# Performance work log

Measured on AMD Instinct MI355X. Metric: run time of the kernel, lower is better.

The kernel has to match this reference:

```python
import jax, jax.numpy as jnp
import numpy as np

B = 256        # batch_size
T = 256        # max_length
H = 1024       # hidden width (hardcoded in module)
NOISE = 128    # noise_depth
NOUT = 100     # n_outputs
EPS = 1e-5     # BatchNorm1d default eps
SLOPE = 0.01   # LeakyReLU default negative_slope


def _bn(x, g, b):
    # BatchNorm1d in training mode: biased batch stats over dim 0
    m = jnp.mean(x, axis=0)
    v = jnp.var(x, axis=0)
    return (x - m) * jax.lax.rsqrt(v + EPS) * g + b


def setup_inputs() -> dict:
    key = jax.random.key(0)
    ks = jax.random.split(key, 16)
    s = 0.02
    d = {
        "z": jax.random.normal(ks[0], (B, NOISE), jnp.float32),
        # projection linears (torch Linear weight layout: [out, in])
        "W_zh": jax.random.normal(ks[1], (H, NOISE), jnp.float32) * s,
        "b_zh": jnp.zeros((H,), jnp.float32),
        "W_zc": jax.random.normal(ks[2], (H, NOISE), jnp.float32) * s,
        "b_zc": jnp.zeros((H,), jnp.float32),
        # BN affine params (torch default init: gamma=1, beta=0)
        "g_bnzh": jnp.ones((H,), jnp.float32), "b_bnzh": jnp.zeros((H,), jnp.float32),
        "g_bnzc": jnp.ones((H,), jnp.float32), "b_bnzc": jnp.zeros((H,), jnp.float32),
        # LSTMCell params, gate order i,f,g,o
        "W_ih": jax.random.normal(ks[3], (4 * H, H), jnp.float32) * s,
        "b_ih": jnp.zeros((4 * H,), jnp.float32),
        "W_hh": jax.random.normal(ks[4], (4 * H, H), jnp.float32) * s,
        "b_hh": jnp.zeros((4 * H,), jnp.float32),
        "g_bn0": jnp.ones((H,), jnp.float32), "b_bn0": jnp.zeros((H,), jnp.float32),
        "W1": jax.random.normal(ks[5], (512, H), jnp.float32) * s,
        "b1": jnp.zeros((512,), jnp.float32),
        "g_bn1": jnp.ones((512,), jnp.float32), "b_bn1": jnp.zeros((512,), jnp.float32),
        "W2": jax.random.normal(ks[6], (256, 512), jnp.float32) * s,
        "b2": jnp.zeros((256,), jnp.float32),
        "g_bn2": jnp.ones((256,), jnp.float32), "b_bn2": jnp.zeros((256,), jnp.float32),
        "W3": jax.random.normal(ks[7], (NOUT, 256), jnp.float32) * s,
        "b3": jnp.zeros((NOUT,), jnp.float32),
        # 'go' token: one-hot [1,0,...,0] tiled over batch
        "go": jnp.zeros((B, H), jnp.float32).at[:, 0].set(1.0),
    }
    return d


def reference(z, W_zh, b_zh, W_zc, b_zc, g_bnzh, b_bnzh, g_bnzc, b_bnzc,
              W_ih, b_ih, W_hh, b_hh, g_bn0, b_bn0, W1, b1, g_bn1, b_bn1,
              W2, b2, g_bn2, b_bn2, W3, b3, go):
    zh = _bn(z @ W_zh.T + b_zh, g_bnzh, b_bnzh)   # initial h
    zc = _bn(z @ W_zc.T + b_zc, g_bnzc, b_bnzc)   # initial c

    def step(carry, _):
        h, c, x = carry
        gates = x @ W_ih.T + b_ih + h @ W_hh.T + b_hh  # [B, 4H]
        i, f, g, o = jnp.split(gates, 4, axis=1)
        c2 = jax.nn.sigmoid(f) * c + jax.nn.sigmoid(i) * jnp.tanh(g)
        h2 = jax.nn.sigmoid(o) * jnp.tanh(c2)
        return (h2, c2, h2), h2  # next input is h2 (out = hx)

    _, ys = jax.lax.scan(step, (zh, zc, go), None, length=T)  # ys: [T, B, H]

    # torch: output = stack(dim=2) -> [B, H, T]; then view(-1, H) on raw memory
    output = jnp.transpose(ys, (1, 2, 0))          # [B, H, T] contiguous
    output_stack = output.reshape(-1, H)           # faithful raw reshape (mixes H and T)

    o1 = jax.nn.leaky_relu(_bn(output_stack, g_bn0, b_bn0) @ W1.T + b1, SLOPE)
    o2 = jax.nn.leaky_relu(_bn(o1, g_bn1, b_bn1) @ W2.T + b2, SLOPE)
    o3 = _bn(o2, g_bn2, b_bn2) @ W3.T + b3          # [B*T*?, NOUT] flat

    output_unstack = o3.reshape(B, -1, T)           # [B, NOUT, T]
    return jax.nn.softmax(output_unstack, axis=1)
```

## Files before the change

kernel.cpp:

```cpp
#include <hip/hip_runtime.h>
#include <hip/hip_bf16.h>

typedef __attribute__((ext_vector_type(8))) short bf16x8;
typedef __attribute__((ext_vector_type(4))) float f32x4;

#define NBLK 256

__device__ inline unsigned short f2b(float x){
  union { float f; unsigned int u; } v; v.f = x;
  unsigned int u = v.u;
  return (unsigned short)((u + 0x7FFFu + ((u >> 16) & 1u)) >> 16);
}
__device__ inline float b2f(unsigned short h){
  union { unsigned int u; float f; } v; v.u = ((unsigned int)h) << 16; return v.f;
}
__device__ inline float sigm(float x){ return 1.f / (1.f + __expf(-x)); }
__device__ inline float tanh_f(float x){ float e2 = __expf(2.f * x); return 1.f - 2.f / (e2 + 1.f); }

__global__ __launch_bounds__(256) void zerofill(float* __restrict__ p, int n){
  int i = blockIdx.x * 256 + threadIdx.x;
  if (i < n) p[i] = 0.f;
}

__device__ inline int packrow(int n){
  int g = n >> 10, h = n & 1023;
  return (h >> 3) * 32 + (h & 7) * 4 + g;
}

__global__ __launch_bounds__(256) void prep_w(
    const float* __restrict__ Wih, const float* __restrict__ Whh,
    const float* __restrict__ bih, const float* __restrict__ bhh,
    unsigned short* __restrict__ Wsum_p, unsigned short* __restrict__ Whh_b,
    float* __restrict__ bias_sp)
{
  size_t idx = (size_t)blockIdx.x * 256 + threadIdx.x;
  int n = (int)(idx >> 10), k = (int)(idx & 1023);
  int g = n >> 10, h = n & 1023;
  float wi = Wih[idx], wh = Whh[idx];
  int htile = h >> 3;
  int r  = ((h & 7) << 2) | g;
  int nt = r >> 4, lr2 = r & 15;
  int kb = k >> 5, lg2 = (k >> 3) & 3, e = k & 7;
  size_t dest = (size_t)htile * 32768 + (size_t)nt * 16384 + (size_t)kb * 512
              + (size_t)(lg2 * 16 + lr2) * 8 + e;
  Wsum_p[dest] = f2b(wi + wh);
  Whh_b[idx] = f2b(wh);
  if (idx < 4096) bias_sp[packrow((int)idx)] = bih[idx] + bhh[idx];
}

__global__ __launch_bounds__(256) void prep_b0(
    const float* __restrict__ Wih, const float* __restrict__ go,
    const float* __restrict__ bih, const float* __restrict__ bhh,
    float* __restrict__ bias0)
{
  __shared__ float red[4];
  int n = blockIdx.x, t = threadIdx.x;
  float acc = 0.f;
  for (int k = t; k < 1024; k += 256) acc += Wih[(size_t)n*1024 + k] * go[k];
  for (int off = 32; off > 0; off >>= 1) acc += __shfl_down(acc, off, 64);
  if ((t & 63) == 0) red[t >> 6] = acc;
  __syncthreads();
  if (t == 0) bias0[n] = bih[n] + bhh[n] + red[0] + red[1] + red[2] + red[3];
}

__global__ __launch_bounds__(256) void zproj(
    const float* __restrict__ z, const float* __restrict__ Wzh, const float* __restrict__ bzh,
    const float* __restrict__ Wzc, const float* __restrict__ bzc,
    float* __restrict__ zh_raw, float* __restrict__ zc_raw)
{
  int idx = blockIdx.x * 256 + threadIdx.x;
  int b = idx >> 10, c = idx & 1023;
  const float* zr = z + b * 128;
  const float* wh = Wzh + c * 128;
  const float* wc = Wzc + c * 128;
  float s1 = bzh[c], s2 = bzc[c];
  #pragma unroll 8
  for (int k = 0; k < 128; k++){ float zv = zr[k]; s1 += zv * wh[k]; s2 += zv * wc[k]; }
  zh_raw[idx] = s1; zc_raw[idx] = s2;
}

__global__ __launch_bounds__(256) void bn_init(
    const float* __restrict__ zh_raw, const float* __restrict__ zc_raw,
    const float* __restrict__ g_h, const float* __restrict__ bt_h,
    const float* __restrict__ g_c, const float* __restrict__ bt_c,
    unsigned short* __restrict__ zh_b, float* __restrict__ c_f)
{
  __shared__ float red[4][4];
  int c = blockIdx.x, r = threadIdx.x;
  float v1 = zh_raw[r * 1024 + c];
  float v2 = zc_raw[r * 1024 + c];
  float s[4] = { v1, v1*v1, v2, v2*v2 };
  #pragma unroll
  for (int i = 0; i < 4; i++){
    float x = s[i];
    for (int off = 32; off > 0; off >>= 1) x += __shfl_down(x, off, 64);
    if ((r & 63) == 0) red[i][r >> 6] = x;
  }
  __syncthreads();
  float m1 = (red[0][0]+red[0][1]+red[0][2]+red[0][3]) * (1.f/256.f);
  float q1 = (red[1][0]+red[1][1]+red[1][2]+red[1][3]) * (1.f/256.f);
  float m2 = (red[2][0]+red[2][1]+red[2][2]+red[2][3]) * (1.f/256.f);
  float q2 = (red[3][0]+red[3][1]+red[3][2]+red[3][3]) * (1.f/256.f);
  float var1 = q1 - m1*m1; if (var1 < 0.f) var1 = 0.f;
  float var2 = q2 - m2*m2; if (var2 < 0.f) var2 = 0.f;
  float a1 = g_h[c] * rsqrtf(var1 + 1e-5f), be1 = bt_h[c] - m1*a1;
  float a2 = g_c[c] * rsqrtf(var2 + 1e-5f), be2 = bt_c[c] - m2*a2;
  zh_b[r * 1024 + c] = f2b(v1*a1 + be1);
  c_f[r * 1024 + c] = v2*a2 + be2;
}

template<int K, int ACT, int OBF16>
__global__ __launch_bounds__(256) void gemm_bt2(
    const unsigned short* __restrict__ A, const unsigned short* __restrict__ B,
    const float* __restrict__ bias, void* __restrict__ outp, int N)
{
  const int tid = threadIdx.x;
  const int w = tid >> 6, l = tid & 63;
  const int lr = l & 15, lg = l >> 4;
  const int m0 = blockIdx.y * 64 + (w >> 1) * 32;
  const int n0 = blockIdx.x * 128 + (w & 1) * 64;
  f32x4 acc[2][4];
  #pragma unroll
  for (int i = 0; i < 2; i++)
    #pragma unroll
    for (int j = 0; j < 4; j++) acc[i][j] = (f32x4){0.f,0.f,0.f,0.f};

  const unsigned short* pa0 = A + (size_t)(m0 + lr) * K + lg * 8;
  const unsigned short* pa1 = pa0 + (size_t)16 * K;
  const unsigned short* pb0 = B + (size_t)(n0 + lr) * K + lg * 8;

  for (int kb = 0; kb < K; kb += 32){
    bf16x8 a0 = *(const bf16x8*)(pa0 + kb);
    bf16x8 a1 = *(const bf16x8*)(pa1 + kb);
    bf16x8 b0 = *(const bf16x8*)(pb0 + kb);
    bf16x8 b1 = *(const bf16x8*)(pb0 + (size_t)16 * K + kb);
    bf16x8 b2 = *(const bf16x8*)(pb0 + (size_t)32 * K + kb);
    bf16x8 b3 = *(const bf16x8*)(pb0 + (size_t)48 * K + kb);
    acc[0][0] = __builtin_amdgcn_mfma_f32_16x16x32_bf16(a0, b0, acc[0][0], 0, 0, 0);
    acc[0][1] = __builtin_amdgcn_mfma_f32_16x16x32_bf16(a0, b1, acc[0][1], 0, 0, 0);
    acc[0][2] = __builtin_amdgcn_mfma_f32_16x16x32_bf16(a0, b2, acc[0][2], 0, 0, 0);
    acc[0][3] = __builtin_amdgcn_mfma_f32_16x16x32_bf16(a0, b3, acc[0][3], 0, 0, 0);
    acc[1][0] = __builtin_amdgcn_mfma_f32_16x16x32_bf16(a1, b0, acc[1][0], 0, 0, 0);
    acc[1][1] = __builtin_amdgcn_mfma_f32_16x16x32_bf16(a1, b1, acc[1][1], 0, 0, 0);
    acc[1][2] = __builtin_amdgcn_mfma_f32_16x16x32_bf16(a1, b2, acc[1][2], 0, 0, 0);
    acc[1][3] = __builtin_amdgcn_mfma_f32_16x16x32_bf16(a1, b3, acc[1][3], 0, 0, 0);
  }

  #pragma unroll
  for (int mi = 0; mi < 2; mi++)
    #pragma unroll
    for (int ni = 0; ni < 4; ni++){
      int col = n0 + ni * 16 + lr;
      float bs = bias[col];
      #pragma unroll
      for (int j = 0; j < 4; j++){
        int row = m0 + mi * 16 + lg * 4 + j;
        float v = acc[mi][ni][j] + bs;
        if (ACT) v = v > 0.f ? v : 0.01f * v;
        if (OBF16) ((unsigned short*)outp)[(size_t)row * N + col] = f2b(v);
        else       ((float*)outp)[(size_t)row * N + col] = v;
      }
    }
}

__global__ __launch_bounds__(256) void lstm_cell0(
    const float* __restrict__ gates, float* __restrict__ c,
    unsigned short* __restrict__ hbuf0)
{
  int idx = blockIdx.x * 256 + threadIdx.x;
  int b = idx >> 10, h = idx & 1023;
  const float* g = gates + (size_t)b * 4096;
  float ig = g[h], fg = g[1024 + h], gg = g[2048 + h], og = g[3072 + h];
  float co = c[idx];
  float c2 = sigm(fg) * co + sigm(ig) * tanh_f(gg);
  float h2 = sigm(og) * tanh_f(c2);
  c[idx] = c2;
  hbuf0[idx] = f2b(h2);
}

__global__ __launch_bounds__(512, 1) void lstm_persist(
    const unsigned short* __restrict__ Wp, const float* __restrict__ bias_sp,
    unsigned short* __restrict__ hbuf0, unsigned short* __restrict__ hbuf1,
    const float* __restrict__ c_init, unsigned short* __restrict__ ys,
    unsigned int* __restrict__ arr, unsigned int* __restrict__ rel)
{
  __shared__ unsigned short Wl[32768];
  __shared__ unsigned short chunk[1024][20];
  const int tid = threadIdx.x;
  const int blk = blockIdx.x;
  const int mhalf = blk >> 7;
  const int htile = blk & 127;
  const int w = tid >> 6, l = tid & 63;
  const int lr = l & 15, lg = l >> 4;
  const int m0 = mhalf * 128;
  const int halfbase = mhalf << 7;
  const int lid = blk - halfbase;
  const bool leader = (lid < 2);

  {
    const bf16x8* src = (const bf16x8*)(Wp + (size_t)htile * 32768);
    bf16x8* dst = (bf16x8*)Wl;
    for (int i = tid; i < 4096; i += 512) dst[i] = src[i];
  }
  for (int i = tid; i < 1024; i += 512){
    int b = i >> 3, hl = i & 7;
    chunk[i][0] = hbuf0[(size_t)(m0 + b) * 1024 + htile * 8 + hl];
  }

  const int hw0 = lr >> 2;
  float bb[2];
  bb[0] = bias_sp[htile * 32 + lr];
  bb[1] = bias_sp[htile * 32 + 16 + lr];

  float creg[2][4];
  #pragma unroll
  for (int ni = 0; ni < 2; ni++)
    #pragma unroll
    for (int j = 0; j < 4; j++){
      int row = m0 + w * 16 + lg * 4 + j;
      int h = htile * 8 + ni * 4 + hw0;
      creg[ni][j] = c_init[(size_t)row * 1024 + h];
    }

  __syncthreads();

  const char* lwb = (const char*)Wl + l * 16;

  #pragma unroll 1
  for (int t = 1; t < 256; t++){
    const unsigned short* hin = (t & 1) ? hbuf0 : hbuf1;
    unsigned long long* hout64 = (unsigned long long*)((t & 1) ? hbuf1 : hbuf0);

    f32x4 acc[2];
    acc[0] = (f32x4){0.f,0.f,0.f,0.f};
    acc[1] = (f32x4){0.f,0.f,0.f,0.f};

    const unsigned short* pa0 = hin + (size_t)(m0 + w * 16 + lr) * 1024 + lg * 8;

    #pragma unroll 8
    for (int kb = 0; kb < 32; kb++){
      bf16x8 a0 = *(const bf16x8*)(pa0 + kb * 32);
      bf16x8 b0 = *(const bf16x8*)(lwb + kb * 1024);
      bf16x8 b1 = *(const bf16x8*)(lwb + 32768 + kb * 1024);
      acc[0] = __builtin_amdgcn_mfma_f32_16x16x32_bf16(a0, b0, acc[0], 0, 0, 0);
      acc[1] = __builtin_amdgcn_mfma_f32_16x16x32_bf16(a0, b1, acc[1], 0, 0, 0);
    }

    #pragma unroll
    for (int ni = 0; ni < 2; ni++)
      #pragma unroll
      for (int j = 0; j < 4; j++){
        float v = acc[ni][j] + bb[ni];
        float va = v;
        float vb = __shfl_xor(v, 1);
        float vc = __shfl_xor(v, 2);
        float vd = __shfl_xor(vb, 2);
        bool s1 = (lr & 1), s2 = (lr & 2);
        float P1 = s2 ? vc : va, P2 = s2 ? vd : vb;
        float Q1 = s2 ? va : vc, Q2 = s2 ? vb : vd;
        float gi  = s1 ? P2 : P1;
        float gf  = s1 ? P1 : P2;
        float gg  = s1 ? Q2 : Q1;
        float go_ = s1 ? Q1 : Q2;
        float c2 = sigm(gf) * creg[ni][j] + sigm(gi) * tanh_f(gg);
        float h2 = sigm(go_) * tanh_f(c2);
        creg[ni][j] = c2;
        unsigned short hb = f2b(h2);
        int rl = w * 16 + lg * 4 + j;
        int hl = ni * 4 + hw0;
        if ((lr & 3) == 0) chunk[rl * 8 + hl][t & 15] = hb;
        unsigned int u0 = (unsigned int)hb
                        | ((unsigned int)(unsigned short)__shfl_xor((int)hb, 4) << 16);
        unsigned long long v64 = (unsigned long long)u0
                               | ((unsigned long long)(unsigned int)__shfl_xor((int)u0, 8) << 32);
        if ((lr & 15) == 1)
          atomicExch(&hout64[(size_t)(m0 + rl) * 256 + htile * 2 + ni], v64);
      }

    __syncthreads();
    if (t < 255 && tid == 0){
      __hip_atomic_fetch_add(&arr[blk * 32], 1u, __ATOMIC_RELAXED, __HIP_MEMORY_SCOPE_AGENT);
      __builtin_amdgcn_fence(__ATOMIC_ACQUIRE, "agent");
    }

    if ((t & 15) == 15){
      int t0 = t - 15;
      for (int r = tid; r < 1024; r += 512){
        int b = r >> 3, hl = r & 7;
        uint2 p0 = *(const uint2*)&chunk[r][0];
        uint2 p1 = *(const uint2*)&chunk[r][4];
        uint2 p2 = *(const uint2*)&chunk[r][8];
        uint2 p3 = *(const uint2*)&chunk[r][12];
        size_t o = ((size_t)(m0 + b) * 1024 + htile * 8 + hl) * 256 + t0;
        *(uint4*)&ys[o]     = (uint4){p0.x, p0.y, p1.x, p1.y};
        *(uint4*)&ys[o + 8] = (uint4){p2.x, p2.y, p3.x, p3.y};
      }
    }

    if (t < 255){
      if (leader){
        if (tid < 128){
          int spin = 0;
          while (__hip_atomic_fetch_add(&arr[(halfbase + tid) * 32], 0u,
                                        __ATOMIC_RELAXED, __HIP_MEMORY_SCOPE_AGENT)
                     < (unsigned)t
                 && spin < (1 << 16)){
            __builtin_amdgcn_s_sleep(1);
            ++spin;
          }
        }
        __syncthreads();
        if (tid < 64)
          __hip_atomic_fetch_add(&rel[(halfbase + lid * 64 + tid) * 32], 1u,
                                 __ATOMIC_RELAXED, __HIP_MEMORY_SCOPE_AGENT);
      } else {
        if (tid == 0){
          int spin = 0;
          while (__hip_atomic_fetch_add(&rel[blk * 32], 0u,
                                        __ATOMIC_RELAXED, __HIP_MEMORY_SCOPE_AGENT)
                     < (unsigned)t
                 && spin < (1 << 16)){
            __builtin_amdgcn_s_sleep(1);
            ++spin;
          }
        }
      }
      __syncthreads();
    }
  }
}

template<int C>
__global__ __launch_bounds__(256) void stats1(
    const unsigned short* __restrict__ X, float* __restrict__ psum, float* __restrict__ psq)
{
  int col = blockIdx.x * 256 + threadIdx.x;
  int r0 = blockIdx.y * 256;
  float s = 0.f, q = 0.f;
  for (int r = r0; r < r0 + 256; r++){
    float v = b2f(X[(size_t)r * C + col]);
    s += v; q += v * v;
  }
  psum[(size_t)blockIdx.y * C + col] = s;
  psq [(size_t)blockIdx.y * C + col] = q;
}

__global__ __launch_bounds__(256) void stats2(
    const float* __restrict__ psum, const float* __restrict__ psq,
    const float* __restrict__ g, const float* __restrict__ b,
    float* __restrict__ alpha, float* __restrict__ beta, int C)
{
  int c = blockIdx.x * 256 + threadIdx.x;
  if (c >= C) return;
  float s = 0.f, q = 0.f;
  for (int i = 0; i < 256; i++){ s += psum[(size_t)i * C + c]; q += psq[(size_t)i * C + c]; }
  float m = s * (1.f / 65536.f);
  float var = q * (1.f / 65536.f) - m * m; if (var < 0.f) var = 0.f;
  float a = g[c] * rsqrtf(var + 1e-5f);
  alpha[c] = a; beta[c] = b[c] - m * a;
}

template<int K>
__global__ __launch_bounds__(256) void foldk(
    const float* __restrict__ W, const float* __restrict__ bias,
    const float* __restrict__ alpha, const float* __restrict__ beta,
    unsigned short* __restrict__ Wb, float* __restrict__ bp, int rows)
{
  __shared__ float red[4];
  int o = blockIdx.x, t = threadIdx.x;
  float acc = 0.f;
  if (o < rows){
    for (int j = t; j < K; j += 256){
      float wv = W[(size_t)o * K + j];
      acc += beta[j] * wv;
      Wb[(size_t)o * K + j] = f2b(wv * alpha[j]);
    }
  } else {
    for (int j = t; j < K; j += 256) Wb[(size_t)o * K + j] = 0;
  }
  for (int off = 32; off > 0; off >>= 1) acc += __shfl_down(acc, off, 64);
  if ((t & 63) == 0) red[t >> 6] = acc;
  __syncthreads();
  if (t == 0) bp[o] = (o < rows ? bias[o] : 0.f) + red[0] + red[1] + red[2] + red[3];
}

__global__ __launch_bounds__(256) void softmax_k(
    const unsigned short* __restrict__ o3p, float* __restrict__ out)
{
  __shared__ unsigned short tile[25600];
  int b = blockIdx.x, t = threadIdx.x;
  const unsigned short* src = o3p + (size_t)b * 256 * 128;
  for (int i = t; i < 25600; i += 256){
    int rr = i / 100, nc = i - rr * 100;
    tile[i] = src[rr * 128 + nc];
  }
  __syncthreads();
  int v = t;
  float mx = -1e30f;
  for (int u = 0; u < 100; u++) mx = fmaxf(mx, b2f(tile[u * 256 + v]));
  float s = 0.f;
  for (int u = 0; u < 100; u++) s += __expf(b2f(tile[u * 256 + v]) - mx);
  float inv = 1.f / s;
  float* dst = out + (size_t)b * 25600;
  for (int u = 0; u < 100; u++)
    dst[u * 256 + v] = __expf(b2f(tile[u * 256 + v]) - mx) * inv;
}

extern "C" void kernel_launch(void* const* d_in, const int* in_sizes, int n_in,
                              void* d_out, int out_size, void* d_ws, size_t ws_size,
                              hipStream_t stream)
{
  (void)in_sizes; (void)n_in;
  const float* z     = (const float*)d_in[0];
  const float* Wzh   = (const float*)d_in[1];
  const float* bzh   = (const float*)d_in[2];
  const float* Wzc   = (const float*)d_in[3];
  const float* bzc   = (const float*)d_in[4];
  const float* g_bnzh= (const float*)d_in[5];
  const float* b_bnzh= (const float*)d_in[6];
  const float* g_bnzc= (const float*)d_in[7];
  const float* b_bnzc= (const float*)d_in[8];
  const float* Wih   = (const float*)d_in[9];
  const float* bih   = (const float*)d_in[10];
  const float* Whh   = (const float*)d_in[11];
  const float* bhh   = (const float*)d_in[12];
  const float* g_bn0 = (const float*)d_in[13];
  const float* b_bn0 = (const float*)d_in[14];
  const float* W1    = (const float*)d_in[15];
  const float* b1    = (const float*)d_in[16];
  const float* g_bn1 = (const float*)d_in[17];
  const float* b_bn1 = (const float*)d_in[18];
  const float* W2    = (const float*)d_in[19];
  const float* b2    = (const float*)d_in[20];
  const float* g_bn2 = (const float*)d_in[21];
  const float* b_bn2 = (const float*)d_in[22];
  const float* W3    = (const float*)d_in[23];
  const float* b3    = (const float*)d_in[24];
  const float* go    = (const float*)d_in[25];

  char* base = (char*)d_ws;
  size_t off = 0;
  auto alloc = [&](size_t bytes)->char*{
    char* p = base + off;
    off = (off + bytes + 255) & ~(size_t)255;
    return p;
  };
  const size_t MB = 1024 * 1024;

  unsigned short* ys = (unsigned short*)alloc(128 * MB);
  unsigned short* o1 = (unsigned short*)alloc(64 * MB);
  char* zone = alloc(32 * MB);
  unsigned short* Wsum_p = (unsigned short*)(zone);
  unsigned short* Whh_b  = (unsigned short*)(zone + 8 * MB);
  float*          gates0 = (float*)(zone + 16 * MB);
  float* zh_raw = (float*)alloc(1 * MB);
  float* zc_raw = (float*)alloc(1 * MB);
  float* bias_sp = (float*)alloc(16384);
  float* bias0   = (float*)alloc(16384);
  unsigned short* zh_b  = (unsigned short*)alloc((size_t)256 * 1024 * 2);
  unsigned short* hbuf0 = (unsigned short*)alloc((size_t)256 * 1024 * 2);
  unsigned short* hbuf1 = (unsigned short*)alloc((size_t)256 * 1024 * 2);
  float* c_f    = (float*)alloc((size_t)256 * 1024 * 4);
  float* psum   = (float*)alloc(1 * MB);
  float* psq    = (float*)alloc(1 * MB);
  float* alpha0 = (float*)alloc(4096); float* beta0 = (float*)alloc(4096);
  float* alpha1 = (float*)alloc(4096); float* beta1 = (float*)alloc(4096);
  float* alpha2 = (float*)alloc(4096); float* beta2 = (float*)alloc(4096);
  unsigned short* W1b = (unsigned short*)alloc((size_t)512 * 1024 * 2);
  unsigned short* W2b = (unsigned short*)alloc((size_t)256 * 512 * 2);
  unsigned short* W3b = (unsigned short*)alloc((size_t)128 * 256 * 2);
  float* b1p = (float*)alloc(4096);
  float* b2p = (float*)alloc(4096);
  float* b3p = (float*)alloc(4096);
  unsigned int* arr = (unsigned int*)alloc(32768);
  unsigned int* rel = (unsigned int*)alloc(32768);
  unsigned short* o2  = (unsigned short*)zone;
  unsigned short* o3p = o1;

  if (off > ws_size){
    zerofill<<<(out_size + 255) / 256, 256, 0, stream>>>((float*)d_out, out_size);
    return;
  }

  zerofill<<<64, 256, 0, stream>>>((float*)arr, 16384);
  prep_w<<<16384, 256, 0, stream>>>(Wih, Whh, bih, bhh, Wsum_p, Whh_b, bias_sp);
  prep_b0<<<4096, 256, 0, stream>>>(Wih, go, bih, bhh, bias0);
  zproj<<<1024, 256, 0, stream>>>(z, Wzh, bzh, Wzc, bzc, zh_raw, zc_raw);
  bn_init<<<1024, 256, 0, stream>>>(zh_raw, zc_raw, g_bnzh, b_bnzh, g_bnzc, b_bnzc, zh_b, c_f);

  gemm_bt2<1024, 0, 0><<<dim3(32, 4), 256, 0, stream>>>(zh_b, Whh_b, bias0, gates0, 4096);
  lstm_cell0<<<1024, 256, 0, stream>>>(gates0, c_f, hbuf0);

  lstm_persist<<<NBLK, 512, 0, stream>>>(Wsum_p, bias_sp, hbuf0, hbuf1, c_f, ys, arr, rel);

  stats1<1024><<<dim3(4, 256), 256, 0, stream>>>(ys, psum, psq);
  stats2<<<4, 256, 0, stream>>>(psum, psq, g_bn0, b_bn0, alpha0, beta0, 1024);
  foldk<1024><<<512, 256, 0, stream>>>(W1, b1, alpha0, beta0, W1b, b1p, 512);
  gemm_bt2<1024, 1, 1><<<dim3(4, 1024), 256, 0, stream>>>(ys, W1b, b1p, o1, 512);

  stats1<512><<<dim3(2, 256), 256, 0, stream>>>(o1, psum, psq);
  stats2<<<2, 256, 0, stream>>>(psum, psq, g_bn1, b_bn1, alpha1, beta1, 512);
  foldk<512><<<256, 256, 0, stream>>>(W2, b2, alpha1, beta1, W2b, b2p, 256);
  gemm_bt2<512, 1, 1><<<dim3(2, 1024), 256, 0, stream>>>(o1, W2b, b2p, o2, 256);

  stats1<256><<<dim3(1, 256), 256, 0, stream>>>(o2, psum, psq);
  stats2<<<1, 256, 0, stream>>>(psum, psq, g_bn2, b_bn2, alpha2, beta2, 256);
  foldk<256><<<128, 256, 0, stream>>>(W3, b3, alpha2, beta2, W3b, b3p, 100);
  gemm_bt2<256, 0, 1><<<dim3(1, 1024), 256, 0, stream>>>(o2, W3b, b3p, o3p, 128);

  softmax_k<<<256, 256, 0, stream>>>(o3p, (float*)d_out);
}
```

Baseline: 4.041 ms.

## Replace global step barrier with per-group readiness flags and a polling wave

Removes the two-level arrive/release grid barrier in the persistent LSTM kernel. Each block now counts its arrival in one of 8 group counters per batch half and adds a ninth wave that polls those counters. The compute waves start each K-chunk of the recurrent matmul as soon as the matching group of h-tiles is ready. The h state becomes a 4-deep ring buffer so producers can run ahead without overwriting inputs still being read. This lets compute overlap with waiting and shortens the barrier's critical path, at the cost of an extra wave per block and LDS spin loops.

Result: slower. 4.410 ms (+9.1%).

```diff
diff --git a/kernel.cpp b/kernel.cpp
--- a/kernel.cpp
+++ b/kernel.cpp
@@ -16,6 +16,13 @@
 }
 __device__ inline float sigm(float x){ return 1.f / (1.f + __expf(-x)); }
 __device__ inline float tanh_f(float x){ float e2 = __expf(2.f * x); return 1.f - 2.f / (e2 + 1.f); }
+
+__device__ inline unsigned apoll(unsigned int* p){
+  return __hip_atomic_fetch_add(p, 0u, __ATOMIC_RELAXED, __HIP_MEMORY_SCOPE_AGENT);
+}
+__device__ inline void aadd(unsigned int* p){
+  __hip_atomic_fetch_add(p, 1u, __ATOMIC_RELAXED, __HIP_MEMORY_SCOPE_AGENT);
+}
 
 __global__ __launch_bounds__(256) void zerofill(float* __restrict__ p, int n){
   int i = blockIdx.x * 256 + threadIdx.x;
@@ -178,14 +185,16 @@
   hbuf0[idx] = f2b(h2);
 }
 
-__global__ __launch_bounds__(512, 1) void lstm_persist(
+__global__ __launch_bounds__(576, 1) void lstm_persist(
     const unsigned short* __restrict__ Wp, const float* __restrict__ bias_sp,
-    unsigned short* __restrict__ hbuf0, unsigned short* __restrict__ hbuf1,
-    const float* __restrict__ c_init, unsigned short* __restrict__ ys,
-    unsigned int* __restrict__ arr, unsigned int* __restrict__ rel)
+    unsigned short* __restrict__ hbufs, const float* __restrict__ c_init,
+    unsigned short* __restrict__ ys, unsigned int* __restrict__ grp)
 {
   __shared__ unsigned short Wl[32768];
   __shared__ unsigned short chunk[1024][20];
+  __shared__ unsigned ready_f[8];
+  __shared__ unsigned bail_f;
+
   const int tid = threadIdx.x;
   const int blk = blockIdx.x;
   const int mhalf = blk >> 7;
@@ -193,19 +202,18 @@
   const int w = tid >> 6, l = tid & 63;
   const int lr = l & 15, lg = l >> 4;
   const int m0 = mhalf * 128;
-  const int halfbase = mhalf << 7;
-  const int lid = blk - halfbase;
-  const bool leader = (lid < 2);
 
   {
     const bf16x8* src = (const bf16x8*)(Wp + (size_t)htile * 32768);
     bf16x8* dst = (bf16x8*)Wl;
-    for (int i = tid; i < 4096; i += 512) dst[i] = src[i];
-  }
-  for (int i = tid; i < 1024; i += 512){
+    for (int i = tid; i < 4096; i += 576) dst[i] = src[i];
+  }
+  for (int i = tid; i < 1024; i += 576){
     int b = i >> 3, hl = i & 7;
-    chunk[i][0] = hbuf0[(size_t)(m0 + b) * 1024 + htile * 8 + hl];
-  }
+    chunk[i][0] = hbufs[(size_t)(m0 + b) * 1024 + htile * 8 + hl];
+  }
+  if (tid < 8) ready_f[tid] = 0;
+  if (tid == 8) bail_f = 0;
 
   const int hw0 = lr >> 2;
   float bb[2];
@@ -213,77 +221,98 @@
   bb[1] = bias_sp[htile * 32 + 16 + lr];
 
   float creg[2][4];
-  #pragma unroll
-  for (int ni = 0; ni < 2; ni++)
-    #pragma unroll
-    for (int j = 0; j < 4; j++){
-      int row = m0 + w * 16 + lg * 4 + j;
-      int h = htile * 8 + ni * 4 + hw0;
-      creg[ni][j] = c_init[(size_t)row * 1024 + h];
-    }
-
-  __syncthreads();
-
-  const char* lwb = (const char*)Wl + l * 16;
-
-  #pragma unroll 1
-  for (int t = 1; t < 256; t++){
-    const unsigned short* hin = (t & 1) ? hbuf0 : hbuf1;
-    unsigned long long* hout64 = (unsigned long long*)((t & 1) ? hbuf1 : hbuf0);
-
-    f32x4 acc[2];
-    acc[0] = (f32x4){0.f,0.f,0.f,0.f};
-    acc[1] = (f32x4){0.f,0.f,0.f,0.f};
-
-    const unsigned short* pa0 = hin + (size_t)(m0 + w * 16 + lr) * 1024 + lg * 8;
-
-    #pragma unroll 8
-    for (int kb = 0; kb < 32; kb++){
-      bf16x8 a0 = *(const bf16x8*)(pa0 + kb * 32);
-      bf16x8 b0 = *(const bf16x8*)(lwb + kb * 1024);
-      bf16x8 b1 = *(const bf16x8*)(lwb + 32768 + kb * 1024);
-      acc[0] = __builtin_amdgcn_mfma_f32_16x16x32_bf16(a0, b0, acc[0], 0, 0, 0);
-      acc[1] = __builtin_amdgcn_mfma_f32_16x16x32_bf16(a0, b1, acc[1], 0, 0, 0);
-    }
-
+  if (w < 8){
     #pragma unroll
     for (int ni = 0; ni < 2; ni++)
       #pragma unroll
       for (int j = 0; j < 4; j++){
-        float v = acc[ni][j] + bb[ni];
-        float va = v;
-        float vb = __shfl_xor(v, 1);
-        float vc = __shfl_xor(v, 2);
-        float vd = __shfl_xor(vb, 2);
-        bool s1 = (lr & 1), s2 = (lr & 2);
-        float P1 = s2 ? vc : va, P2 = s2 ? vd : vb;
-        float Q1 = s2 ? va : vc, Q2 = s2 ? vb : vd;
-        float gi  = s1 ? P2 : P1;
-        float gf  = s1 ? P1 : P2;
-        float gg  = s1 ? Q2 : Q1;
-        float go_ = s1 ? Q1 : Q2;
-        float c2 = sigm(gf) * creg[ni][j] + sigm(gi) * tanh_f(gg);
-        float h2 = sigm(go_) * tanh_f(c2);
-        creg[ni][j] = c2;
-        unsigned short hb = f2b(h2);
-        int rl = w * 16 + lg * 4 + j;
-        int hl = ni * 4 + hw0;
-        if ((lr & 3) == 0) chunk[rl * 8 + hl][t & 15] = hb;
-        unsigned int u0 = (unsigned int)hb
-                        | ((unsigned int)(unsigned short)__shfl_xor((int)hb, 4) << 16);
-        unsigned long long v64 = (unsigned long long)u0
-                               | ((unsigned long long)(unsigned int)__shfl_xor((int)u0, 8) << 32);
-        if ((lr & 15) == 1)
-          atomicExch(&hout64[(size_t)(m0 + rl) * 256 + htile * 2 + ni], v64);
+        int row = m0 + w * 16 + lg * 4 + j;
+        int h = htile * 8 + ni * 4 + hw0;
+        creg[ni][j] = c_init[(size_t)row * 1024 + h];
       }
+  }
+
+  __syncthreads();
+
+  const char* lwb = (const char*)Wl + l * 16;
+  volatile unsigned* rdy = ready_f;
+  volatile unsigned* bl  = &bail_f;
+
+  #pragma unroll 1
+  for (int t = 1; t < 256; t++){
+    const unsigned short* hin = hbufs + (size_t)((t - 1) & 3) * 262144;
+    unsigned long long* hout64 = (unsigned long long*)(hbufs + (size_t)(t & 3) * 262144);
+
+    if (w == 8){
+      __builtin_amdgcn_fence(__ATOMIC_ACQUIRE, "agent");
+      if (l < 8){
+        unsigned tgt = 16u * (unsigned)(t - 1);
+        int spin = 0;
+        while (apoll(&grp[(mhalf * 8 + l) * 32]) < tgt && !(*bl)){
+          if (++spin > (1 << 14)){ *bl = 1; break; }
+          __builtin_amdgcn_s_sleep(1);
+        }
+        rdy[l] = (unsigned)t;
+      }
+    } else {
+      f32x4 acc[2];
+      acc[0] = (f32x4){0.f,0.f,0.f,0.f};
+      acc[1] = (f32x4){0.f,0.f,0.f,0.f};
+      const unsigned short* pa0 = hin + (size_t)(m0 + w * 16 + lr) * 1024 + lg * 8;
+
+      #pragma unroll 1
+      for (int g = 0; g < 8; g++){
+        { int spin = 0;
+          while (rdy[g] < (unsigned)t && !(*bl)){ if (++spin > (1 << 20)){ *bl = 1; break; } } }
+        __builtin_amdgcn_sched_barrier(0);
+        #pragma unroll
+        for (int kk = 0; kk < 4; kk++){
+          int kb = g * 4 + kk;
+          bf16x8 a0 = *(const bf16x8*)(pa0 + kb * 32);
+          bf16x8 b0 = *(const bf16x8*)(lwb + kb * 1024);
+          bf16x8 b1 = *(const bf16x8*)(lwb + 32768 + kb * 1024);
+          acc[0] = __builtin_amdgcn_mfma_f32_16x16x32_bf16(a0, b0, acc[0], 0, 0, 0);
+          acc[1] = __builtin_amdgcn_mfma_f32_16x16x32_bf16(a0, b1, acc[1], 0, 0, 0);
+        }
+      }
+
+      #pragma unroll
+      for (int ni = 0; ni < 2; ni++)
+        #pragma unroll
+        for (int j = 0; j < 4; j++){
+          float v = acc[ni][j] + bb[ni];
+          float va = v;
+          float vb = __shfl_xor(v, 1);
+          float vc = __shfl_xor(v, 2);
+          float vd = __shfl_xor(vb, 2);
+          bool s1 = (lr & 1), s2 = (lr & 2);
+          float P1 = s2 ? vc : va, P2 = s2 ? vd : vb;
+          float Q1 = s2 ? va : vc, Q2 = s2 ? vb : vd;
+          float gi  = s1 ? P2 : P1;
+          float gf  = s1 ? P1 : P2;
+          float gg  = s1 ? Q2 : Q1;
+          float go_ = s1 ? Q1 : Q2;
+          float c2 = sigm(gf) * creg[ni][j] + sigm(gi) * tanh_f(gg);
+          float h2 = sigm(go_) * tanh_f(c2);
+          creg[ni][j] = c2;
+          unsigned short hb = f2b(h2);
+          int rl = w * 16 + lg * 4 + j;
+          int hl = ni * 4 + hw0;
+          if ((lr & 3) == 0) chunk[rl * 8 + hl][t & 15] = hb;
+          unsigned int u0 = (unsigned int)hb
+                          | ((unsigned int)(unsigned short)__shfl_xor((int)hb, 4) << 16);
+          unsigned long long v64 = (unsigned long long)u0
+                                 | ((unsigned long long)(unsigned int)__shfl_xor((int)u0, 8) << 32);
+          if ((lr & 15) == 1)
+            atomicExch(&hout64[(size_t)(m0 + rl) * 256 + htile * 2 + ni], v64);
+        }
+    }
 
     __syncthreads();
-    if (t < 255 && tid == 0){
-      __hip_atomic_fetch_add(&arr[blk * 32], 1u, __ATOMIC_RELAXED, __HIP_MEMORY_SCOPE_AGENT);
-      __builtin_amdgcn_fence(__ATOMIC_ACQUIRE, "agent");
-    }
-
-    if ((t & 15) == 15){
+
+    if (w == 8){
+      if (l == 0 && t < 255) aadd(&grp[(mhalf * 8 + (htile >> 4)) * 32]);
+    } else if ((t & 15) == 15){
       int t0 = t - 15;
       for (int r = tid; r < 1024; r += 512){
         int b = r >> 3, hl = r & 7;
@@ -297,36 +326,7 @@
       }
     }
 
-    if (t < 255){
-      if (leader){
-        if (tid < 128){
-          int spin = 0;
-          while (__hip_atomic_fetch_add(&arr[(halfbase + tid) * 32], 0u,
-                                        __ATOMIC_RELAXED, __HIP_MEMORY_SCOPE_AGENT)
-                     < (unsigned)t
-                 && spin < (1 << 16)){
-            __builtin_amdgcn_s_sleep(1);
-            ++spin;
-          }
-        }
-        __syncthreads();
-        if (tid < 64)
-          __hip_atomic_fetch_add(&rel[(halfbase + lid * 64 + tid) * 32], 1u,
-                                 __ATOMIC_RELAXED, __HIP_MEMORY_SCOPE_AGENT);
-      } else {
-        if (tid == 0){
-          int spin = 0;
-          while (__hip_atomic_fetch_add(&rel[blk * 32], 0u,
-                                        __ATOMIC_RELAXED, __HIP_MEMORY_SCOPE_AGENT)
-                     < (unsigned)t
-                 && spin < (1 << 16)){
-            __builtin_amdgcn_s_sleep(1);
-            ++spin;
-          }
-        }
-      }
-      __syncthreads();
-    }
+    __syncthreads();
   }
 }
 
@@ -458,8 +458,7 @@
   float* bias_sp = (float*)alloc(16384);
   float* bias0   = (float*)alloc(16384);
   unsigned short* zh_b  = (unsigned short*)alloc((size_t)256 * 1024 * 2);
-  unsigned short* hbuf0 = (unsigned short*)alloc((size_t)256 * 1024 * 2);
-  unsigned short* hbuf1 = (unsigned short*)alloc((size_t)256 * 1024 * 2);
+  unsigned short* hbufs = (unsigned short*)alloc((size_t)4 * 256 * 1024 * 2);
   float* c_f    = (float*)alloc((size_t)256 * 1024 * 4);
   float* psum   = (float*)alloc(1 * MB);
   float* psq    = (float*)alloc(1 * MB);
@@ -472,8 +471,7 @@
   float* b1p = (float*)alloc(4096);
   float* b2p = (float*)alloc(4096);
   float* b3p = (float*)alloc(4096);
-  unsigned int* arr = (unsigned int*)alloc(32768);
-  unsigned int* rel = (unsigned int*)alloc(32768);
+  unsigned int* grp = (unsigned int*)alloc(2048);
   unsigned short* o2  = (unsigned short*)zone;
   unsigned short* o3p = o1;
 
@@ -482,16 +480,16 @@
     return;
   }
 
-  zerofill<<<64, 256, 0, stream>>>((float*)arr, 16384);
+  zerofill<<<2, 256, 0, stream>>>((float*)grp, 512);
   prep_w<<<16384, 256, 0, stream>>>(Wih, Whh, bih, bhh, Wsum_p, Whh_b, bias_sp);
   prep_b0<<<4096, 256, 0, stream>>>(Wih, go, bih, bhh, bias0);
   zproj<<<1024, 256, 0, stream>>>(z, Wzh, bzh, Wzc, bzc, zh_raw, zc_raw);
   bn_init<<<1024, 256, 0, stream>>>(zh_raw, zc_raw, g_bnzh, b_bnzh, g_bnzc, b_bnzc, zh_b, c_f);
 
   gemm_bt2<1024, 0, 0><<<dim3(32, 4), 256, 0, stream>>>(zh_b, Whh_b, bias0, gates0, 4096);
-  lstm_cell0<<<1024, 256, 0, stream>>>(gates0, c_f, hbuf0);
-
-  lstm_persist<<<NBLK, 512, 0, stream>>>(Wsum_p, bias_sp, hbuf0, hbuf1, c_f, ys, arr, rel);
+  lstm_cell0<<<1024, 256, 0, stream>>>(gates0, c_f, hbufs);
+
+  lstm_persist<<<NBLK, 576, 0, stream>>>(Wsum_p, bias_sp, hbufs, c_f, ys, grp);
 
   stats1<1024><<<dim3(4, 256), 256, 0, stream>>>(ys, psum, psq);
   stats2<<<4, 256, 0, stream>>>(psum, psq, g_bn0, b_bn0, alpha0, beta0, 1024);
```
